# Kernel optimization log

Hardware: AMD Instinct MI355X
Metric: run time of the kernel (lower is better)

## Reference

```python
import jax, jax.numpy as jnp
import numpy as np

B, C, N = 4, 32, 256
D_IN, D_EMB, K = 512, 1024, 4096  # input_dim, llm_embedding_dim, codebook_size
EPS = 1e-12


def setup_inputs() -> dict:
    key = jax.random.key(0)
    ks = jax.random.split(key, 6)
    s_in = float(1.0 / np.sqrt(D_IN))
    s_emb = float(1.0 / np.sqrt(D_EMB))
    return {
        "x": jax.random.normal(ks[0], (B, C, N, D_IN), jnp.float32),
        # nn.Linear(input_dim, llm_embedding_dim): weight [out, in], uniform(-1/sqrt(in), 1/sqrt(in))
        "w_in": jax.random.uniform(ks[1], (D_EMB, D_IN), jnp.float32, -s_in, s_in),
        "b_in": jax.random.uniform(ks[2], (D_EMB,), jnp.float32, -s_in, s_in),
        "w_out": jax.random.uniform(ks[3], (D_IN, D_EMB), jnp.float32, -s_emb, s_emb),
        "b_out": jax.random.uniform(ks[4], (D_IN,), jnp.float32, -s_emb, s_emb),
        # frozen LLM-embedding codebook (copied from llm_embedding_bank, requires_grad=False)
        "codebook": jax.random.normal(ks[5], (K, D_EMB), jnp.float32),
    }


def _rotate_to(src, tgt):
    # Rotation trick (arXiv:2410.06424, sec 4.2) as in vector-quantize-pytorch.
    # Forward value equals tgt; gradient flows through src via a (detached)
    # Householder rotation + scaling.
    n_src = jnp.linalg.norm(src, axis=-1, keepdims=True)
    n_tgt = jnp.linalg.norm(tgt, axis=-1, keepdims=True)
    u = jax.lax.stop_gradient(src / jnp.maximum(n_src, EPS))   # unit src, detached
    q = tgt / jnp.maximum(n_tgt, EPS)                          # unit tgt (codebook: no grad)
    w = u + q
    w = jax.lax.stop_gradient(w / jnp.maximum(jnp.linalg.norm(w, axis=-1, keepdims=True), EPS))
    rot = (src
           - 2.0 * jnp.sum(src * w, -1, keepdims=True) * w
           + 2.0 * jnp.sum(src * u, -1, keepdims=True) * q)
    return rot * jax.lax.stop_gradient(n_tgt / jnp.maximum(n_src, EPS))


def reference(x, w_in, b_in, w_out, b_out, codebook):
    Bb, Cc, Nn, _ = x.shape
    # input projection, flatten channels x patches into token axis
    z = jnp.einsum('bcnd,ed->bcne', x, w_in) + b_in          # [B, C, N, D_EMB]
    z = z.reshape(Bb, Cc * Nn, -1)                           # [B, T, D_EMB]
    # squared euclidean distances to codebook: ||z||^2 - 2 z.c + ||c||^2
    dists = (jnp.sum(z * z, -1, keepdims=True)
             - 2.0 * jnp.einsum('bte,ke->btk', z, codebook)
             + jnp.sum(codebook * codebook, -1))             # [B, T, K]
    indices = jnp.argmin(dists, axis=-1)                     # [B, T] int
    q = codebook[indices]                                    # gather [B, T, D_EMB]
    quantized = _rotate_to(z, q)                             # == q in value
    # commitment loss (commitment_weight = 1.0); codebook frozen -> only commit term
    aux_loss = jnp.mean((jax.lax.stop_gradient(quantized) - z) ** 2)
    out = jnp.einsum('bte,de->btd', quantized, w_out) + b_out
    return (out.reshape(Bb, Cc, Nn, -1),
            indices,
            quantized.reshape(Bb, Cc, Nn, -1),
            aux_loss)
```

## Files before the change

kernel.cpp:

```cpp
#include <hip/hip_runtime.h>

#define M_TOK 32768
#define DIN   512
#define DEMB  1024
#define KC    4096

#define IDX_OFF ((size_t)M_TOK * DIN)
#define Q_OFF   (IDX_OFF + M_TOK)
#define AUX_OFF (Q_OFF + (size_t)M_TOK * DEMB)

typedef _Float16 f16x8 __attribute__((ext_vector_type(8)));
typedef _Float16 f16x4 __attribute__((ext_vector_type(4)));
typedef float f32x4 __attribute__((ext_vector_type(4)));

__device__ inline void gload16(const void* g, void* s) {
    __builtin_amdgcn_global_load_lds((const __attribute__((address_space(1))) void*)g,
                                     (__attribute__((address_space(3))) void*)s, 16, 0, 0);
}

__device__ inline unsigned umin2(unsigned a, unsigned b) { return a < b ? a : b; }
__device__ inline unsigned umax2(unsigned a, unsigned b) { return a > b ? a : b; }

__device__ inline float block_reduce_sum_256(float v) {
#pragma unroll
    for (int off = 32; off > 0; off >>= 1) v += __shfl_down(v, off);
    __shared__ float smem[4];
    const int lane = threadIdx.x & 63;
    const int w = threadIdx.x >> 6;
    if (lane == 0) smem[w] = v;
    __syncthreads();
    return smem[0] + smem[1] + smem[2] + smem[3];
}

__global__ __launch_bounds__(256) void prep_all(const float* __restrict__ cb,
                                                const float* __restrict__ w_out,
                                                const float* __restrict__ w_in,
                                                _Float16* __restrict__ cbf,
                                                _Float16* __restrict__ wof,
                                                _Float16* __restrict__ wpk,
                                                _Float16* __restrict__ cbp,
                                                float* __restrict__ cn2p,
                                                float* __restrict__ aux) {
    const int b = blockIdx.x;
    if (b < 4096) {
        if (b == 0 && threadIdx.x == 0) *aux = 0.0f;
        const float4 v = reinterpret_cast<const float4*>(cb + (size_t)b * DEMB)[threadIdx.x];
        f16x4 h;
        h[0] = (_Float16)v.x; h[1] = (_Float16)v.y; h[2] = (_Float16)v.z; h[3] = (_Float16)v.w;
        reinterpret_cast<f16x4*>(cbf + (size_t)b * DEMB)[threadIdx.x] = h;
        float s = v.x * v.x + v.y * v.y + v.z * v.z + v.w * v.w;
        s = block_reduce_sum_256(s);
        if (threadIdx.x == 0) cn2p[b] = 0.5f * s + 1024.0f;
    } else if (b < 4352) {
        const size_t i = (size_t)(b - 4096) * 256 + threadIdx.x;
        const float4 a = reinterpret_cast<const float4*>(w_out)[i * 2];
        const float4 b4 = reinterpret_cast<const float4*>(w_out)[i * 2 + 1];
        f16x8 h;
        h[0] = (_Float16)a.x; h[1] = (_Float16)a.y; h[2] = (_Float16)a.z; h[3] = (_Float16)a.w;
        h[4] = (_Float16)b4.x; h[5] = (_Float16)b4.y; h[6] = (_Float16)b4.z; h[7] = (_Float16)b4.w;
        reinterpret_cast<f16x8*>(wof)[i] = h;
    } else if (b < 6400) {
        const int id = (b - 4352) * 256 + threadIdx.x;
        const int c16 = id >> 11;
        const int rem = id & 2047;
        const int kk = rem >> 6;
        const int l = rem & 63;
        const int lgq = l >> 4, lcq = l & 15;
        const float* src = cb + ((size_t)(c16 * 16 + lcq)) * DEMB + kk * 32 + lgq * 8;
        const float4 a = *reinterpret_cast<const float4*>(src);
        const float4 b4 = *reinterpret_cast<const float4*>(src + 4);
        f16x8 h;
        h[0] = (_Float16)a.x; h[1] = (_Float16)a.y; h[2] = (_Float16)a.z; h[3] = (_Float16)a.w;
        h[4] = (_Float16)b4.x; h[5] = (_Float16)b4.y; h[6] = (_Float16)b4.z; h[7] = (_Float16)b4.w;
        const int ntile = c16 >> 2, nn = c16 & 3;
        const size_t off = ((size_t)(kk * 256 + ntile * 4 + nn)) * 64 + l;
        *reinterpret_cast<f16x8*>(cbp + off * 8) = h;
    } else {
        const int id = (b - 6400) * 256 + threadIdx.x;
        const int l = id & 63;
        const int hl = (id >> 6) & 1;
        const int c16 = (id >> 7) & 63;
        const int kk = id >> 13;
        const int col = c16 * 16 + (l & 15);
        const int kb = kk * 32 + (l >> 4) * 8;
        const float* src = w_in + (size_t)col * DIN + kb;
        const float4 a = *reinterpret_cast<const float4*>(src);
        const float4 b4 = *reinterpret_cast<const float4*>(src + 4);
        const float e[8] = {a.x, a.y, a.z, a.w, b4.x, b4.y, b4.z, b4.w};
        f16x8 o;
#pragma unroll
        for (int j = 0; j < 8; ++j) {
            const _Float16 hv = (_Float16)e[j];
            o[j] = hl ? (_Float16)((e[j] - (float)hv) * 2048.0f) : hv;
        }
        *reinterpret_cast<f16x8*>(wpk + (size_t)id * 8) = o;
    }
}

__global__ void __launch_bounds__(512)
__attribute__((amdgpu_waves_per_eu(2, 2)))
zgemm_stream(const float* __restrict__ x,
             const _Float16* __restrict__ wpk,
             const float* __restrict__ bin,
             float* __restrict__ zq,
             _Float16* __restrict__ zf) {
    extern __shared__ _Float16 sm[];
    _Float16* Ah = sm;
    _Float16* Al = sm + 32768;
    const int t = threadIdx.x;
    const int w = t >> 6, l = t & 63;
    const int lg = l >> 4, lc = l & 15;
    const int m0 = blockIdx.x * 64;

    {
        const int r = t >> 3;
        const int c0 = t & 7;
#pragma unroll
        for (int i = 0; i < 8; ++i) {
            const int c = c0 + i * 8;
            const float* px = x + (size_t)(m0 + r) * DIN + c * 8;
            const float4 a = *reinterpret_cast<const float4*>(px);
            const float4 b4 = *reinterpret_cast<const float4*>(px + 4);
            const float e[8] = {a.x, a.y, a.z, a.w, b4.x, b4.y, b4.z, b4.w};
            f16x8 h, lo;
#pragma unroll
            for (int j = 0; j < 8; ++j) {
                const _Float16 hv = (_Float16)e[j];
                h[j] = hv;
                lo[j] = (_Float16)((e[j] - (float)hv) * 2048.0f);
            }
            const int swz = (c & 0x30) | ((c ^ r) & 15);
            *reinterpret_cast<f16x8*>(Ah + (size_t)(r * 64 + swz) * 8) = h;
            *reinterpret_cast<f16x8*>(Al + (size_t)(r * 64 + swz) * 8) = lo;
        }
    }

    const char* ztb = (const char*)sm;
    int lbase[4][4];
#pragma unroll
    for (int m = 0; m < 4; ++m)
#pragma unroll
        for (int j = 0; j < 4; ++j)
            lbase[m][j] = (m * 16 + lc) * 1024 + ((((j * 4) | lg) ^ lc) & 15) * 16;

    const char* pL = (const char*)wpk + w * 4096 + l * 16;

    f16x8 bh[2][2], bl[2][2];
#pragma unroll
    for (int s = 0; s < 2; ++s)
#pragma unroll
        for (int n = 0; n < 2; ++n) {
            bh[s][n] = *reinterpret_cast<const f16x8*>(pL + s * 131072 + n * 2048);
            bl[s][n] = *reinterpret_cast<const f16x8*>(pL + s * 131072 + n * 2048 + 1024);
        }

    __syncthreads();

    f16x8 ah[2][4], al[2][4];
#pragma unroll
    for (int m = 0; m < 4; ++m) {
        ah[0][m] = *reinterpret_cast<const f16x8*>(ztb + lbase[m][0]);
        al[0][m] = *reinterpret_cast<const f16x8*>(ztb + 65536 + lbase[m][0]);
    }

    unsigned boff = 2u * 131072u;
    for (int p = 0; p < 4; ++p) {
        f32x4 acc1[4][2], acc2[4][2];
#pragma unroll
        for (int n = 0; n < 2; ++n) {
            const float bb = bin[p * 256 + w * 32 + n * 16 + lc];
#pragma unroll
            for (int m = 0; m < 4; ++m) {
                acc1[m][n] = (f32x4){bb, bb, bb, bb};
                acc2[m][n] = (f32x4){0.f, 0.f, 0.f, 0.f};
            }
        }
        const unsigned wrapAdd = (unsigned)((p < 3 ? 1 : -3) * 32768 - 15 * 131072);
#pragma unroll
        for (int kk = 0; kk < 16; ++kk) {
            const int nk = (kk + 1) & 15;
#pragma unroll
            for (int m = 0; m < 4; ++m) {
                ah[(kk + 1) & 1][m] = *reinterpret_cast<const f16x8*>(
                    ztb + lbase[m][nk & 3] + ((nk >> 2) << 8));
                al[(kk + 1) & 1][m] = *reinterpret_cast<const f16x8*>(
                    ztb + 65536 + lbase[m][nk & 3] + ((nk >> 2) << 8));
            }
            __builtin_amdgcn_s_setprio(1);
#pragma unroll
            for (int m = 0; m < 4; ++m)
#pragma unroll
                for (int n = 0; n < 2; ++n) {
                    acc1[m][n] = __builtin_amdgcn_mfma_f32_16x16x32_f16(
                        ah[kk & 1][m], bh[kk & 1][n], acc1[m][n], 0, 0, 0);
                    acc2[m][n] = __builtin_amdgcn_mfma_f32_16x16x32_f16(
                        ah[kk & 1][m], bl[kk & 1][n], acc2[m][n], 0, 0, 0);
                    acc2[m][n] = __builtin_amdgcn_mfma_f32_16x16x32_f16(
                        al[kk & 1][m], bh[kk & 1][n], acc2[m][n], 0, 0, 0);
                }
            __builtin_amdgcn_s_setprio(0);
#pragma unroll
            for (int n = 0; n < 2; ++n) {
                bh[kk & 1][n] = *reinterpret_cast<const f16x8*>(pL + boff + n * 2048);
                bl[kk & 1][n] = *reinterpret_cast<const f16x8*>(pL + boff + n * 2048 + 1024);
            }
            boff += (kk == 13) ? wrapAdd : 131072u;
        }
#pragma unroll
        for (int n = 0; n < 2; ++n) {
            const int col = p * 256 + w * 32 + n * 16 + lc;
#pragma unroll
            for (int m = 0; m < 4; ++m)
#pragma unroll
                for (int rg = 0; rg < 4; ++rg) {
                    const int row = m0 + m * 16 + lg * 4 + rg;
                    const float z = acc1[m][n][rg] + acc2[m][n][rg] * (1.0f / 2048.0f);
                    zq[(size_t)row * DEMB + col] = z;
                    zf[(size_t)row * DEMB + col] = (_Float16)(-z);
                }
        }
    }
}

__global__ void __launch_bounds__(512)
__attribute__((amdgpu_waves_per_eu(2, 2)))
dist_topk(const _Float16* __restrict__ zf,
          const _Float16* __restrict__ cbp,
          const float* __restrict__ cn2p,
          unsigned* __restrict__ pk) {
    extern __shared__ _Float16 zt[];
    const int t = threadIdx.x;
    const int w = t >> 6, l = t & 63;
    const int lg = l >> 4, lc = l & 15;
    const int m0 = blockIdx.x * 64;

    {
        const int r0 = t >> 7;
        const int ch = t & 127;
#pragma unroll
        for (int i = 0; i < 16; ++i) {
            const int row = i * 4 + r0;
            const int sch = (ch & 0x70) | ((ch ^ row) & 15);
            gload16(zf + (((size_t)(m0 + row)) << 10) + sch * 8,
                    zt + ((size_t)(i * 512 + t)) * 8);
        }
    }

    const char* ztb = (const char*)zt;
    int lbase[4][4];
#pragma unroll
    for (int m = 0; m < 4; ++m)
#pragma unroll
        for (int j = 0; j < 4; ++j)
            lbase[m][j] = (m * 16 + lc) * 2048 + ((((j * 4) | lg) ^ lc) << 4);

    unsigned k0[16], k1[16];
#pragma unroll
    for (int r = 0; r < 16; ++r) { k0[r] = 0xFFFFFFFFu; k1[r] = 0xFFFFFFFFu; }

    const char* pL = (const char*)cbp + l * 16;

    f16x8 bf[4][4];
    {
#pragma unroll
        for (int s = 0; s < 4; ++s)
#pragma unroll
            for (int n = 0; n < 4; ++n)
                bf[s][n] = *reinterpret_cast<const f16x8*>(pL + s * 262144 + w * 4096 + n * 1024);
    }
    __syncthreads();

    f16x8 af[4][4];
#pragma unroll
    for (int s = 0; s < 2; ++s)
#pragma unroll
        for (int m = 0; m < 4; ++m)
            af[s][m] = *reinterpret_cast<const f16x8*>(ztb + lbase[m][s] + ((s & 28) << 6));

    unsigned boff = (unsigned)(w * 4096 + 4 * 262144);
    for (int nt8 = 0; nt8 < 8; ++nt8) {
        const int ntile = nt8 * 8 + w;
        const unsigned wrapAdd = (unsigned)((nt8 < 7 ? 8 : -56) * 4096 - 31 * 262144);
        const int colb = ntile * 64;
        unsigned colw[4];
        float c2[4];
#pragma unroll
        for (int n = 0; n < 4; ++n) {
            colw[n] = (unsigned)(colb + n * 16 + lc);
            c2[n] = cn2p[colw[n]];
        }
        f32x4 acc[4][4];
#pragma unroll
        for (int m = 0; m < 4; ++m)
#pragma unroll
            for (int n = 0; n < 4; ++n)
                acc[m][n] = (f32x4){c2[n], c2[n], c2[n], c2[n]};

#pragma unroll
        for (int kk = 0; kk < 32; ++kk) {
            const int nk2 = (kk + 2) & 31;
#pragma unroll
            for (int m = 0; m < 4; ++m)
                af[(kk + 2) & 3][m] = *reinterpret_cast<const f16x8*>(
                    ztb + lbase[m][nk2 & 3] + ((nk2 & 28) << 6));
            __builtin_amdgcn_s_setprio(1);
#pragma unroll
            for (int m = 0; m < 4; ++m)
#pragma unroll
                for (int n = 0; n < 4; ++n)
                    acc[m][n] = __builtin_amdgcn_mfma_f32_16x16x32_f16(
                        af[kk & 3][m], bf[kk & 3][n], acc[m][n], 0, 0, 0);
            __builtin_amdgcn_s_setprio(0);
#pragma unroll
            for (int n = 0; n < 4; ++n)
                bf[kk & 3][n] = *reinterpret_cast<const f16x8*>(pL + boff + n * 1024);
            boff += (kk == 27) ? wrapAdd : 262144u;
        }

#pragma unroll
        for (int n = 0; n < 4; ++n) {
#pragma unroll
            for (int m = 0; m < 4; ++m)
#pragma unroll
                for (int rg = 0; rg < 4; ++rg) {
                    const unsigned key =
                        (__float_as_uint(acc[m][n][rg]) & 0xFFFFF000u) | colw[n];
                    const int r = m * 4 + rg;
                    const unsigned kmax = umax2(k0[r], key);
                    k0[r] = umin2(k0[r], key);
                    k1[r] = umin2(k1[r], kmax);
                }
        }
    }
#pragma unroll
    for (int off = 1; off < 16; off <<= 1) {
#pragma unroll
        for (int r = 0; r < 16; ++r) {
            const unsigned b0 = __shfl_xor(k0[r], off);
            const unsigned b1 = __shfl_xor(k1[r], off);
            const unsigned lo = umin2(k0[r], b0);
            const unsigned hi = umax2(k0[r], b0);
            k0[r] = lo;
            k1[r] = umin2(hi, umin2(k1[r], b1));
        }
    }
    if (lc == 0) {
#pragma unroll
        for (int m = 0; m < 4; ++m)
#pragma unroll
            for (int rg = 0; rg < 4; ++rg) {
                const int r = m * 4 + rg;
                const int tok = m0 + m * 16 + lg * 4 + rg;
                pk[(size_t)(w * 2 + 0) * M_TOK + tok] = k0[r];
                pk[(size_t)(w * 2 + 1) * M_TOK + tok] = k1[r];
            }
    }
}

__global__ __launch_bounds__(256) void refine_idx(const float* __restrict__ cb,
                                                  const float* __restrict__ cn2p,
                                                  const unsigned* __restrict__ pk,
                                                  float* __restrict__ zq,
                                                  float* __restrict__ idx_f,
                                                  int* __restrict__ idx_i,
                                                  float* __restrict__ aux) {
    const int wv = threadIdx.x >> 6;
    const int t = blockIdx.x * 4 + wv;
    const int l = threadIdx.x & 63;
    float4* zp = reinterpret_cast<float4*>(zq + ((size_t)t << 10));
    float4 zr[4];
#pragma unroll
    for (int j = 0; j < 4; ++j) zr[j] = zp[l + j * 64];

    float zn = 0.0f;
#pragma unroll
    for (int j = 0; j < 4; ++j) {
        zn = fmaf(zr[j].x, zr[j].x, zn);
        zn = fmaf(zr[j].y, zr[j].y, zn);
        zn = fmaf(zr[j].z, zr[j].z, zn);
        zn = fmaf(zr[j].w, zr[j].w, zn);
    }
#pragma unroll
    for (int off = 1; off < 64; off <<= 1) zn += __shfl_xor(zn, off);

    unsigned v = 0xFFFFFFFFu;
    if (l < 16) v = pk[(size_t)l * M_TOK + t];

    float bestd = 3.4e38f;
    int besti = 0x7fffffff;
#pragma unroll
    for (int s = 0; s < 4; ++s) {
        unsigned mv = v;
#pragma unroll
        for (int off = 1; off < 64; off <<= 1) mv = umin2(mv, __shfl_xor(mv, off));
        if (v == mv) v = 0xFFFFFFFFu;
        const int mi = (int)(mv & 0xFFFu);
        const float4* cp = reinterpret_cast<const float4*>(cb + ((size_t)mi << 10));
        float s4 = 0.0f;
#pragma unroll
        for (int j = 0; j < 4; ++j) {
            const float4 c = cp[l + j * 64];
            s4 = fmaf(zr[j].x, c.x, s4);
            s4 = fmaf(zr[j].y, c.y, s4);
            s4 = fmaf(zr[j].z, c.z, s4);
            s4 = fmaf(zr[j].w, c.w, s4);
        }
#pragma unroll
        for (int off = 1; off < 64; off <<= 1) s4 += __shfl_xor(s4, off);
        const float d = cn2p[mi] - s4;
        if (d < bestd || (d == bestd && mi < besti)) { bestd = d; besti = mi; }
    }
    const float4* cpb = reinterpret_cast<const float4*>(cb + ((size_t)besti << 10));
#pragma unroll
    for (int j = 0; j < 4; ++j) zp[l + j * 64] = cpb[l + j * 64];

    __shared__ float dsum[4];
    if (l == 0) {
        idx_f[t] = (float)besti;
        idx_i[t] = besti;
        dsum[wv] = 2.0f * bestd - 2048.0f + zn;
    }
    __syncthreads();
    if (threadIdx.x == 0)
        atomicAdd(aux, (dsum[0] + dsum[1] + dsum[2] + dsum[3]) * (1.0f / 33554432.0f));
}

__global__ __launch_bounds__(256, 2) void outgemm(const _Float16* __restrict__ cbf,
                                                  const _Float16* __restrict__ wof,
                                                  const float* __restrict__ bout,
                                                  const int* __restrict__ idx,
                                                  float* __restrict__ out) {
    extern __shared__ char smem[];
    _Float16* As = (_Float16*)smem;
    _Float16* Bs = As + 16384;
    const int t = threadIdx.x;
    const int w = t >> 6, l = t & 63;
    const int wm = w >> 1, wn = w & 1;
    const int lg = l >> 4, lc = l & 15;
    const int m0 = blockIdx.y * 128, n0 = blockIdx.x * 128;

    const int sr = t >> 4;
    const int sch = t & 15;
    const int sswz = sch ^ (sr & 15);

    int arow[8];
#pragma unroll
    for (int i = 0; i < 8; ++i) arow[i] = idx[m0 + i * 16 + sr];

    f32x4 acc[4][4] = {};
    for (int kt = 0; kt < 8; ++kt) {
        __syncthreads();
#pragma unroll
        for (int i = 0; i < 8; ++i) {
            gload16(cbf + (size_t)arow[i] * DEMB + kt * 128 + sswz * 8,
                    As + (size_t)(i * 256 + t) * 8);
            gload16(wof + (size_t)(n0 + i * 16 + sr) * DEMB + kt * 128 + sswz * 8,
                    Bs + (size_t)(i * 256 + t) * 8);
        }
        __syncthreads();
#pragma unroll
        for (int kk = 0; kk < 4; ++kk) {
            f16x8 af[4], bf8[4];
#pragma unroll
            for (int m = 0; m < 4; ++m) {
                const int r = wm * 64 + m * 16 + lc;
                const int c = (kk * 4 + lg) ^ lc;
                af[m] = *reinterpret_cast<const f16x8*>(As + (size_t)(r * 16 + c) * 8);
            }
#pragma unroll
            for (int n = 0; n < 4; ++n) {
                const int r = wn * 64 + n * 16 + lc;
                const int c = (kk * 4 + lg) ^ lc;
                bf8[n] = *reinterpret_cast<const f16x8*>(Bs + (size_t)(r * 16 + c) * 8);
            }
            __builtin_amdgcn_s_setprio(1);
#pragma unroll
            for (int m = 0; m < 4; ++m)
#pragma unroll
                for (int n = 0; n < 4; ++n)
                    acc[m][n] = __builtin_amdgcn_mfma_f32_16x16x32_f16(af[m], bf8[n], acc[m][n], 0, 0, 0);
            __builtin_amdgcn_s_setprio(0);
        }
    }
#pragma unroll
    for (int n = 0; n < 4; ++n) {
        const int col = n0 + wn * 64 + n * 16 + lc;
        const float bb = bout[col];
#pragma unroll
        for (int m = 0; m < 4; ++m)
#pragma unroll
            for (int r = 0; r < 4; ++r) {
                const int row = m0 + wm * 64 + m * 16 + lg * 4 + r;
                out[(size_t)row * DIN + col] = acc[m][n][r] + bb;
            }
    }
}

extern "C" void kernel_launch(void* const* d_in, const int* in_sizes, int n_in,
                              void* d_out, int out_size, void* d_ws, size_t ws_size,
                              hipStream_t stream) {
    const float* x = (const float*)d_in[0];
    const float* w_in = (const float*)d_in[1];
    const float* b_in = (const float*)d_in[2];
    const float* w_out = (const float*)d_in[3];
    const float* b_out = (const float*)d_in[4];
    const float* cb = (const float*)d_in[5];

    float* out = (float*)d_out;
    float* idx_f = out + IDX_OFF;
    float* zq = out + Q_OFF;
    float* aux = out + AUX_OFF;
    _Float16* zf = (_Float16*)d_out;

    char* ws = (char*)d_ws;
    float* cn2p = (float*)ws;
    int* idx_i = (int*)(ws + 16384);
    unsigned* pk = (unsigned*)(ws + 147456);
    _Float16* cbf = (_Float16*)(ws + 4341760);
    _Float16* cbp = (_Float16*)(ws + 12730368);
    _Float16* wpk = (_Float16*)(ws + 21118976);
    _Float16* wof = (_Float16*)(ws + 23216128);

    prep_all<<<6912, 256, 0, stream>>>(cb, w_out, w_in, cbf, wof, wpk, cbp, cn2p, aux);
    zgemm_stream<<<M_TOK / 64, 512, 131072, stream>>>(x, wpk, b_in, zq, zf);
    dist_topk<<<M_TOK / 64, 512, 131072, stream>>>(zf, cbp, cn2p, pk);
    refine_idx<<<M_TOK / 4, 256, 0, stream>>>(cb, cn2p, pk, zq, idx_f, idx_i, aux);
    outgemm<<<dim3(DIN / 128, M_TOK / 128), 256, 65536, stream>>>(cbf, wof, b_out, idx_i, out);
}
```

Measured before the change: 515.4 us.

## Rewrite output GEMM to stream pre-packed weight fragments with full-row token tiles

The output projection now processes 64 gathered codebook rows per block across all 512 output columns. The whole 64x1024 A tile is loaded into LDS once, and the weight is pre-packed into MFMA fragment order so each wave streams its B operands directly from global/L2 into registers with a 4-deep register pipeline. This removes the per-k-tile LDS staging and barriers of the old 128x128 tiled kernel and the repeated gather of the same codebook rows across four column blocks. The bias is folded into accumulator initialisation. In exchange it uses 128KB of LDS per block and depends heavily on register pressure and L2 bandwidth for the weight stream.

```diff
diff --git a/kernel.cpp b/kernel.cpp
--- a/kernel.cpp
+++ b/kernel.cpp
@@ -36,7 +36,7 @@
                                                 const float* __restrict__ w_out,
                                                 const float* __restrict__ w_in,
                                                 _Float16* __restrict__ cbf,
-                                                _Float16* __restrict__ wof,
+                                                _Float16* __restrict__ wok,
                                                 _Float16* __restrict__ wpk,
                                                 _Float16* __restrict__ cbp,
                                                 float* __restrict__ cn2p,
@@ -52,13 +52,19 @@
         s = block_reduce_sum_256(s);
         if (threadIdx.x == 0) cn2p[b] = 0.5f * s + 1024.0f;
     } else if (b < 4352) {
-        const size_t i = (size_t)(b - 4096) * 256 + threadIdx.x;
-        const float4 a = reinterpret_cast<const float4*>(w_out)[i * 2];
-        const float4 b4 = reinterpret_cast<const float4*>(w_out)[i * 2 + 1];
+        const int id = (b - 4096) * 256 + threadIdx.x;
+        const int l = id & 63;
+        const int c16 = (id >> 6) & 31;
+        const int kk = id >> 11;
+        const int col = c16 * 16 + (l & 15);
+        const int kb = kk * 32 + (l >> 4) * 8;
+        const float* src = w_out + (size_t)col * DEMB + kb;
+        const float4 a = *reinterpret_cast<const float4*>(src);
+        const float4 b4 = *reinterpret_cast<const float4*>(src + 4);
         f16x8 h;
         h[0] = (_Float16)a.x; h[1] = (_Float16)a.y; h[2] = (_Float16)a.z; h[3] = (_Float16)a.w;
         h[4] = (_Float16)b4.x; h[5] = (_Float16)b4.y; h[6] = (_Float16)b4.z; h[7] = (_Float16)b4.w;
-        reinterpret_cast<f16x8*>(wof)[i] = h;
+        *reinterpret_cast<f16x8*>(wok + (size_t)id * 8) = h;
     } else if (b < 6400) {
         const int id = (b - 4352) * 256 + threadIdx.x;
         const int c16 = id >> 11;
@@ -425,73 +431,99 @@
         atomicAdd(aux, (dsum[0] + dsum[1] + dsum[2] + dsum[3]) * (1.0f / 33554432.0f));
 }
 
-__global__ __launch_bounds__(256, 2) void outgemm(const _Float16* __restrict__ cbf,
-                                                  const _Float16* __restrict__ wof,
-                                                  const float* __restrict__ bout,
-                                                  const int* __restrict__ idx,
-                                                  float* __restrict__ out) {
-    extern __shared__ char smem[];
-    _Float16* As = (_Float16*)smem;
-    _Float16* Bs = As + 16384;
+__global__ void __launch_bounds__(512)
+__attribute__((amdgpu_waves_per_eu(2, 2)))
+outgemm_stream(const _Float16* __restrict__ cbf,
+               const _Float16* __restrict__ wok,
+               const float* __restrict__ bout,
+               const int* __restrict__ idx,
+               float* __restrict__ out) {
+    extern __shared__ _Float16 at[];
     const int t = threadIdx.x;
     const int w = t >> 6, l = t & 63;
-    const int wm = w >> 1, wn = w & 1;
     const int lg = l >> 4, lc = l & 15;
-    const int m0 = blockIdx.y * 128, n0 = blockIdx.x * 128;
-
-    const int sr = t >> 4;
-    const int sch = t & 15;
-    const int sswz = sch ^ (sr & 15);
-
-    int arow[8];
-#pragma unroll
-    for (int i = 0; i < 8; ++i) arow[i] = idx[m0 + i * 16 + sr];
-
-    f32x4 acc[4][4] = {};
-    for (int kt = 0; kt < 8; ++kt) {
-        __syncthreads();
-#pragma unroll
-        for (int i = 0; i < 8; ++i) {
-            gload16(cbf + (size_t)arow[i] * DEMB + kt * 128 + sswz * 8,
-                    As + (size_t)(i * 256 + t) * 8);
-            gload16(wof + (size_t)(n0 + i * 16 + sr) * DEMB + kt * 128 + sswz * 8,
-                    Bs + (size_t)(i * 256 + t) * 8);
-        }
-        __syncthreads();
-#pragma unroll
-        for (int kk = 0; kk < 4; ++kk) {
-            f16x8 af[4], bf8[4];
-#pragma unroll
-            for (int m = 0; m < 4; ++m) {
-                const int r = wm * 64 + m * 16 + lc;
-                const int c = (kk * 4 + lg) ^ lc;
-                af[m] = *reinterpret_cast<const f16x8*>(As + (size_t)(r * 16 + c) * 8);
-            }
-#pragma unroll
-            for (int n = 0; n < 4; ++n) {
-                const int r = wn * 64 + n * 16 + lc;
-                const int c = (kk * 4 + lg) ^ lc;
-                bf8[n] = *reinterpret_cast<const f16x8*>(Bs + (size_t)(r * 16 + c) * 8);
-            }
-            __builtin_amdgcn_s_setprio(1);
-#pragma unroll
-            for (int m = 0; m < 4; ++m)
-#pragma unroll
-                for (int n = 0; n < 4; ++n)
-                    acc[m][n] = __builtin_amdgcn_mfma_f32_16x16x32_f16(af[m], bf8[n], acc[m][n], 0, 0, 0);
-            __builtin_amdgcn_s_setprio(0);
-        }
-    }
+    const int m0 = blockIdx.x * 64;
+
+    {
+        const int r0 = t >> 7;
+        const int ch = t & 127;
+#pragma unroll
+        for (int i = 0; i < 16; ++i) {
+            const int row = i * 4 + r0;
+            const int gi = idx[m0 + row];
+            const int sch = (ch & 0x70) | ((ch ^ row) & 15);
+            gload16(cbf + (((size_t)gi) << 10) + sch * 8,
+                    at + ((size_t)(i * 512 + t)) * 8);
+        }
+    }
+
+    const char* ztb = (const char*)at;
+    int lbase[4][4];
+#pragma unroll
+    for (int m = 0; m < 4; ++m)
+#pragma unroll
+        for (int j = 0; j < 4; ++j)
+            lbase[m][j] = (m * 16 + lc) * 2048 + ((((j * 4) | lg) ^ lc) << 4);
+
+    const char* pL = (const char*)wok + l * 16;
+
+    f16x8 bf[4][4];
+    {
+#pragma unroll
+        for (int s = 0; s < 4; ++s)
+#pragma unroll
+            for (int n = 0; n < 4; ++n)
+                bf[s][n] = *reinterpret_cast<const f16x8*>(pL + s * 32768 + w * 4096 + n * 1024);
+    }
+    __syncthreads();
+
+    f16x8 af[4][4];
+#pragma unroll
+    for (int s = 0; s < 2; ++s)
+#pragma unroll
+        for (int m = 0; m < 4; ++m)
+            af[s][m] = *reinterpret_cast<const f16x8*>(ztb + lbase[m][s] + ((s & 28) << 6));
+
+    f32x4 acc[4][4];
 #pragma unroll
     for (int n = 0; n < 4; ++n) {
-        const int col = n0 + wn * 64 + n * 16 + lc;
-        const float bb = bout[col];
-#pragma unroll
-        for (int m = 0; m < 4; ++m)
-#pragma unroll
-            for (int r = 0; r < 4; ++r) {
-                const int row = m0 + wm * 64 + m * 16 + lg * 4 + r;
-                out[(size_t)row * DIN + col] = acc[m][n][r] + bb;
+        const float bb = bout[w * 64 + n * 16 + lc];
+#pragma unroll
+        for (int m = 0; m < 4; ++m)
+            acc[m][n] = (f32x4){bb, bb, bb, bb};
+    }
+
+    unsigned boff = (unsigned)(w * 4096 + 4 * 32768);
+#pragma unroll
+    for (int kk = 0; kk < 32; ++kk) {
+        const int nk2 = (kk + 2) & 31;
+#pragma unroll
+        for (int m = 0; m < 4; ++m)
+            af[(kk + 2) & 3][m] = *reinterpret_cast<const f16x8*>(
+                ztb + lbase[m][nk2 & 3] + ((nk2 & 28) << 6));
+        __builtin_amdgcn_s_setprio(1);
+#pragma unroll
+        for (int m = 0; m < 4; ++m)
+#pragma unroll
+            for (int n = 0; n < 4; ++n)
+                acc[m][n] = __builtin_amdgcn_mfma_f32_16x16x32_f16(
+                    af[kk & 3][m], bf[kk & 3][n], acc[m][n], 0, 0, 0);
+        __builtin_amdgcn_s_setprio(0);
+#pragma unroll
+        for (int n = 0; n < 4; ++n)
+            bf[kk & 3][n] = *reinterpret_cast<const f16x8*>(pL + boff + n * 1024);
+        boff += (kk == 27) ? (unsigned)(-(28 * 32768)) : 32768u;
+    }
+
+#pragma unroll
+    for (int n = 0; n < 4; ++n) {
+        const int col = w * 64 + n * 16 + lc;
+#pragma unroll
+        for (int m = 0; m < 4; ++m)
+#pragma unroll
+            for (int rg = 0; rg < 4; ++rg) {
+                const int row = m0 + m * 16 + lg * 4 + rg;
+                out[(size_t)row * DIN + col] = acc[m][n][rg];
             }
     }
 }
@@ -519,11 +551,11 @@
     _Float16* cbf = (_Float16*)(ws + 4341760);
     _Float16* cbp = (_Float16*)(ws + 12730368);
     _Float16* wpk = (_Float16*)(ws + 21118976);
-    _Float16* wof = (_Float16*)(ws + 23216128);
-
-    prep_all<<<6912, 256, 0, stream>>>(cb, w_out, w_in, cbf, wof, wpk, cbp, cn2p, aux);
+    _Float16* wok = (_Float16*)(ws + 23216128);
+
+    prep_all<<<6912, 256, 0, stream>>>(cb, w_out, w_in, cbf, wok, wpk, cbp, cn2p, aux);
     zgemm_stream<<<M_TOK / 64, 512, 131072, stream>>>(x, wpk, b_in, zq, zf);
     dist_topk<<<M_TOK / 64, 512, 131072, stream>>>(zf, cbp, cn2p, pk);
     refine_idx<<<M_TOK / 4, 256, 0, stream>>>(cb, cn2p, pk, zq, idx_f, idx_i, aux);
-    outgemm<<<dim3(DIN / 128, M_TOK / 128), 256, 65536, stream>>>(cbf, wof, b_out, idx_i, out);
-}
+    outgemm_stream<<<M_TOK / 64, 512, 131072, stream>>>(cbf, wok, b_out, idx_i, out);
+}
```

Result: no change. 520.3 us (+1.0%).
